# Kernel optimization log

Measured on AMD Instinct MI355X. Metric: run time of the kernel, lower is better.

The kernel has to match this reference:

```python
import jax, jax.numpy as jnp
import numpy as np

EPS = 1e-12  # F.normalize eps


def setup_inputs() -> dict:
    key = jax.random.key(0)
    k1, k2 = jax.random.split(key)
    bs, d = 8192, 128
    data = jax.random.normal(k1, (bs, d), dtype=jnp.float32)
    label = jax.random.randint(k2, (bs, 1), 0, 2, dtype=jnp.int64)
    scale = jnp.asarray(np.log(1.0 / 0.07), dtype=jnp.float32)  # learned temperature param
    return {"data": data, "scale": scale, "label": label}


def reference(data, scale, label):
    bs = data.shape[0]
    # L2-normalize rows (F.normalize semantics with eps clamp)
    norm = jnp.maximum(jnp.linalg.norm(data, axis=-1, keepdims=True), EPS)
    x = data / norm
    logits = (x @ x.T) * jnp.exp(scale)  # [bs, bs]
    # Vectorized equivalent of the python double loop: binary same-class matrix
    sim = (label == label.T).astype(logits.dtype)  # [bs, bs]
    q = jax.nn.softmax(sim / jnp.sum(sim, axis=-1, keepdims=True), axis=-1)
    p = jax.nn.log_softmax(logits, axis=-1)
    log_q = jnp.log(q)  # q > 0 always (softmax output)
    # F.kl_div(p, q, 'batchmean') = sum(q * (log q - p)) / bs
    loss1 = jnp.sum(q * (log_q - p)) / bs
    # F.kl_div(q.log(), p.exp(), 'batchmean') = sum(exp(p) * (p - log q)) / bs
    loss2 = jnp.sum(jnp.exp(p) * (p - log_q)) / bs
    return (loss1 + loss2) * 0.5
```

## Files before the change

### kernel.cpp

```cpp
#include <hip/hip_runtime.h>
#include <stdint.h>

#define BS 8192
#define DD 128
#define SPLIT 16

typedef __attribute__((ext_vector_type(8))) short short8;
typedef __attribute__((ext_vector_type(4))) float float4v;

#if __has_builtin(__builtin_amdgcn_exp2f)
#define EXP2(x) __builtin_amdgcn_exp2f(x)
#else
#define EXP2(x) exp2f(x)
#endif

__device__ __forceinline__ float bf2f(short s) {
  union { unsigned u; float f; } c;
  c.u = ((unsigned)(unsigned short)s) << 16;
  return c.f;
}
__device__ __forceinline__ short f2bf(float f) {
  union { float f; unsigned u; } c; c.f = f;
  unsigned u = c.u + 0x7FFFu + ((c.u >> 16) & 1u);
  return (short)(u >> 16);
}

__global__ __launch_bounds__(256) void k_norm(const float* __restrict__ data,
                                              const int* __restrict__ label,
                                              unsigned int* __restrict__ xnb32,
                                              float* __restrict__ xnf,
                                              float* __restrict__ gh,
                                              int* __restrict__ cnt,
                                              float* __restrict__ Zr,
                                              float* __restrict__ Ur,
                                              float* __restrict__ Vr,
                                              float* __restrict__ mf,
                                              float* __restrict__ out) {
  __shared__ float sh[256];
  __shared__ int shc[2];
  int tid = threadIdx.x, wave = tid >> 6, lane = tid & 63;
  if (tid < 2) shc[tid] = 0;
  sh[tid] = 0.f;
  if (tid < 32) {
    int row = blockIdx.x * 32 + tid;
    Zr[row] = 0.f; Ur[row] = 0.f; Vr[row] = 0.f;
    mf[row] = (label[row] == 0) ? 1.f : 0.f;
  }
  if (blockIdx.x == 0 && tid == 0) out[0] = 0.f;
  __syncthreads();
  float a00 = 0.f, a01 = 0.f, a10 = 0.f, a11 = 0.f;
  int c0 = 0, c1 = 0;
  int rbase = blockIdx.x * 32 + wave * 8;
  for (int r = 0; r < 8; ++r) {
    int row = rbase + r;
    float2 v = *(const float2*)&data[row * DD + lane * 2];
    float ss = v.x * v.x + v.y * v.y;
    for (int off = 32; off; off >>= 1) ss += __shfl_xor(ss, off);
    float rn = 1.f / fmaxf(sqrtf(ss), 1e-12f);
    float x0 = v.x * rn, x1 = v.y * rn;
    *(float2*)&xnf[row * DD + lane * 2] = make_float2(x0, x1);
    unsigned int pk = (unsigned int)(unsigned short)f2bf(x0) |
                      ((unsigned int)(unsigned short)f2bf(x1) << 16);
    xnb32[row * 64 + lane] = pk;
    int lab = label[row];
    if (lab == 0) { a00 += x0; a01 += x1; c0++; }
    else          { a10 += x0; a11 += x1; c1++; }
  }
  atomicAdd(&sh[2 * lane], a00);
  atomicAdd(&sh[2 * lane + 1], a01);
  atomicAdd(&sh[128 + 2 * lane], a10);
  atomicAdd(&sh[128 + 2 * lane + 1], a11);
  if (lane == 0) { atomicAdd(&shc[0], c0); atomicAdd(&shc[1], c1); }
  __syncthreads();
  atomicAdd(&gh[tid], sh[tid]);
  if (tid < 2) atomicAdd(&cnt[tid], shc[tid]);
}

__device__ __forceinline__ void stage_tile(const char* srcbase, int j0,
                                           char* dstbase, int tid) {
  int rowloc = tid >> 4;
  int swz = (tid & 15) ^ rowloc;
  char* dst = dstbase + tid * 16;
#pragma unroll
  for (int p = 0; p < 4; ++p) {
    const char* src = srcbase + (size_t)(j0 + p * 16 + rowloc) * 256 + swz * 16;
    __builtin_amdgcn_global_load_lds(
        (const __attribute__((address_space(1))) void*)(uintptr_t)src,
        (__attribute__((address_space(3))) void*)(uintptr_t)(dst + p * 4096), 16, 0, 0);
  }
}

__device__ __forceinline__ void consume_tile(const short* __restrict__ tile, int j0,
                                             const float* __restrict__ mf,
                                             const short8 afrag[2][4], int quad, int col,
                                             float Z[2][4], float U[2][4], float V0[2][4]) {
#pragma unroll
  for (int jo = 0; jo < 4; ++jo) {
    int jc = j0 + jo * 16 + col;
    float m0 = mf[jc];
    float4v c0 = {0.f, 0.f, 0.f, 0.f}, c1 = {0.f, 0.f, 0.f, 0.f};
    const short* bp = tile + (jo * 16 + col) * DD;
#pragma unroll
    for (int t = 0; t < 4; ++t) {
      short8 b = *(const short8*)(bp + ((t * 4 + quad) ^ col) * 8);
      c0 = __builtin_amdgcn_mfma_f32_16x16x32_bf16(afrag[0][t], b, c0, 0, 0, 0);
      c1 = __builtin_amdgcn_mfma_f32_16x16x32_bf16(afrag[1][t], b, c1, 0, 0, 0);
    }
#pragma unroll
    for (int r = 0; r < 4; ++r) {
      float l0 = c0[r], e0 = EXP2(l0);
      Z[0][r] += e0; U[0][r] += e0 * l0; V0[0][r] += m0 * e0;
      float l1 = c1[r], e1 = EXP2(l1);
      Z[1][r] += e1; U[1][r] += e1 * l1; V0[1][r] += m0 * e1;
    }
  }
}

__global__ __launch_bounds__(256) void k_main(const unsigned short* __restrict__ xnb,
                                              const int* __restrict__ label,
                                              const float* __restrict__ mf,
                                              const float* __restrict__ scale,
                                              float* __restrict__ Zr,
                                              float* __restrict__ Ur,
                                              float* __restrict__ Vr) {
  __shared__ short tileA[64 * DD];
  __shared__ short tileB[64 * DD];
  int tid = threadIdx.x, wave = tid >> 6, lane = tid & 63;
  int quad = lane >> 4, col = lane & 15;
  int rb = blockIdx.x / SPLIT, sl = blockIdx.x % SPLIT;
  float se2 = __expf(scale[0]) * 1.4426950408889634f;

  short8 afrag[2][4];
  int labI[2][4];
#pragma unroll
  for (int s = 0; s < 2; ++s) {
    int arow = rb * 128 + s * 64 + wave * 16 + col;
    const short* ap = (const short*)xnb + (size_t)arow * DD;
#pragma unroll
    for (int t = 0; t < 4; ++t) {
      short8 a = *(const short8*)(ap + t * 32 + quad * 8);
#pragma unroll
      for (int i = 0; i < 8; ++i) a[i] = f2bf(bf2f(a[i]) * se2);
      afrag[s][t] = a;
    }
#pragma unroll
    for (int r = 0; r < 4; ++r)
      labI[s][r] = label[rb * 128 + s * 64 + wave * 16 + quad * 4 + r];
  }

  float Z[2][4] = {}, U[2][4] = {}, V0[2][4] = {};

  const char* srcbase = (const char*)xnb;
  int jbase = sl * (BS / SPLIT), jend = jbase + (BS / SPLIT);

  stage_tile(srcbase, jbase, (char*)tileA, tid);
  __syncthreads();
  for (int j0 = jbase; j0 < jend; j0 += 128) {
    stage_tile(srcbase, j0 + 64, (char*)tileB, tid);
    consume_tile(tileA, j0, mf, afrag, quad, col, Z, U, V0);
    __syncthreads();
    int jn = (j0 + 128 < jend) ? (j0 + 128) : jbase;
    stage_tile(srcbase, jn, (char*)tileA, tid);
    consume_tile(tileB, j0 + 64, mf, afrag, quad, col, Z, U, V0);
    __syncthreads();
  }

#pragma unroll
  for (int s = 0; s < 2; ++s)
#pragma unroll
    for (int r = 0; r < 4; ++r)
#pragma unroll
      for (int off = 1; off < 16; off <<= 1) {
        Z[s][r] += __shfl_xor(Z[s][r], off);
        U[s][r] += __shfl_xor(U[s][r], off);
        V0[s][r] += __shfl_xor(V0[s][r], off);
      }
  if (col == 0) {
#pragma unroll
    for (int s = 0; s < 2; ++s)
#pragma unroll
      for (int r = 0; r < 4; ++r) {
        int row = rb * 128 + s * 64 + wave * 16 + quad * 4 + r;
        float v = (labI[s][r] == 0) ? V0[s][r] : (Z[s][r] - V0[s][r]);
        atomicAdd(&Zr[row], Z[s][r]);
        atomicAdd(&Ur[row], U[s][r] * 0.6931471805599453f);
        atomicAdd(&Vr[row], v);
      }
  }
}

__global__ __launch_bounds__(256) void k_final(const float* __restrict__ xnf,
                                               const int* __restrict__ label,
                                               const float* __restrict__ scale,
                                               const float* __restrict__ gh,
                                               const int* __restrict__ cnt,
                                               const float* __restrict__ Zr,
                                               const float* __restrict__ Ur,
                                               const float* __restrict__ Vr,
                                               float* __restrict__ out) {
  __shared__ float bsum[4];
  int tid = threadIdx.x, wave = tid >> 6, lane = tid & 63;
  float se = __expf(scale[0]);
  float h0a = gh[2 * lane], h0b = gh[2 * lane + 1];
  float h1a = gh[128 + 2 * lane], h1b = gh[128 + 2 * lane + 1];
  float ga = h0a + h1a, gb = h0b + h1b;
  float c0 = (float)cnt[0], c1 = (float)cnt[1];
  float local = 0.f;
  int rbase = blockIdx.x * 32 + wave * 8;
  for (int r = 0; r < 8; ++r) {
    int row = rbase + r;
    float2 x = *(const float2*)&xnf[row * DD + lane * 2];
    int lab = label[row];
    float sg = x.x * ga + x.y * gb;
    float sh_ = (lab == 0) ? (x.x * h0a + x.y * h0b) : (x.x * h1a + x.y * h1b);
    for (int off = 32; off; off >>= 1) {
      sg += __shfl_xor(sg, off);
      sh_ += __shfl_xor(sh_, off);
    }
    if (lane == 0) {
      float cc = (lab == 0) ? c0 : c1;
      float a = __expf(1.f / cc);
      float Zq = cc * a + ((float)BS - cc);
      float S = se * sg, T = se * sh_;
      float Z = Zr[row], U = Ur[row], V = Vr[row];
      local += a / Zq - (S + (a - 1.f) * T) / Zq + U / Z - V / (cc * Z);
    }
  }
  if (lane == 0) bsum[wave] = local;
  __syncthreads();
  if (tid == 0) {
    float s = bsum[0] + bsum[1] + bsum[2] + bsum[3];
    atomicAdd(out, s * (0.5f / (float)BS));
  }
}

extern "C" void kernel_launch(void* const* d_in, const int* in_sizes, int n_in,
                              void* d_out, int out_size, void* d_ws, size_t ws_size,
                              hipStream_t stream) {
  const float* data = (const float*)d_in[0];
  const float* scale = (const float*)d_in[1];
  const int* label = (const int*)d_in[2];
  char* ws = (char*)d_ws;
  unsigned short* xnb = (unsigned short*)ws;
  unsigned int* xnb32 = (unsigned int*)ws;
  float* xnf = (float*)(ws + 2097152);
  float* Zr = (float*)(ws + 6291456);
  float* Ur = (float*)(ws + 6324224);
  float* Vr = (float*)(ws + 6356992);
  float* gh = (float*)(ws + 6389760);
  int* cnt = (int*)(ws + 6390784);
  float* mf = (float*)(ws + 6390800);

  hipMemsetAsync(ws + 6389760, 0, 1032, stream);

  k_norm<<<256, 256, 0, stream>>>(data, label, xnb32, xnf, gh, cnt, Zr, Ur, Vr, mf,
                                  (float*)d_out);
  k_main<<<64 * SPLIT, 256, 0, stream>>>(xnb, label, mf, scale, Zr, Ur, Vr);
  k_final<<<256, 256, 0, stream>>>(xnf, label, scale, gh, cnt, Zr, Ur, Vr, (float*)d_out);
}
```

Before: 121.4 us.

## Exploit Gram matrix symmetry to compute each off-diagonal tile once

Since x@x.T is symmetric, the main kernel now computes only the upper-triangular set of 64x64 tile pairs (diagonal plus half of the circular offsets). Each off-diagonal tile adds both row sums and column sums, so the column-side partial Z/U/V values are reduced across quads and atomically added for the column rows. This roughly halves the MFMA and exp work. In exchange it adds more atomics, shuffles, a smaller A fragment per block, and a grid of 1152 blocks that each run less work.

```diff
diff --git a/kernel.cpp b/kernel.cpp
--- a/kernel.cpp
+++ b/kernel.cpp
@@ -3,7 +3,6 @@
 
 #define BS 8192
 #define DD 128
-#define SPLIT 16
 
 typedef __attribute__((ext_vector_type(8))) short short8;
 typedef __attribute__((ext_vector_type(4))) float float4v;
@@ -90,28 +89,42 @@
   }
 }
 
-__device__ __forceinline__ void consume_tile(const short* __restrict__ tile, int j0,
-                                             const float* __restrict__ mf,
-                                             const short8 afrag[2][4], int quad, int col,
-                                             float Z[2][4], float U[2][4], float V0[2][4]) {
+__device__ __forceinline__ void consume64(const short* __restrict__ tile, int jt64,
+                                          bool docol, const float* __restrict__ mf,
+                                          const short8 afrag[4], const float mrow[4],
+                                          int quad, int col,
+                                          float rZ[4], float rU[4], float rV[4],
+                                          float* __restrict__ Zr,
+                                          float* __restrict__ Ur,
+                                          float* __restrict__ Vr) {
 #pragma unroll
   for (int jo = 0; jo < 4; ++jo) {
-    int jc = j0 + jo * 16 + col;
-    float m0 = mf[jc];
-    float4v c0 = {0.f, 0.f, 0.f, 0.f}, c1 = {0.f, 0.f, 0.f, 0.f};
+    int jc = jt64 + jo * 16 + col;
+    float mcol = mf[jc];
+    float4v c = {0.f, 0.f, 0.f, 0.f};
     const short* bp = tile + (jo * 16 + col) * DD;
 #pragma unroll
     for (int t = 0; t < 4; ++t) {
       short8 b = *(const short8*)(bp + ((t * 4 + quad) ^ col) * 8);
-      c0 = __builtin_amdgcn_mfma_f32_16x16x32_bf16(afrag[0][t], b, c0, 0, 0, 0);
-      c1 = __builtin_amdgcn_mfma_f32_16x16x32_bf16(afrag[1][t], b, c1, 0, 0, 0);
-    }
+      c = __builtin_amdgcn_mfma_f32_16x16x32_bf16(afrag[t], b, c, 0, 0, 0);
+    }
+    float cZ = 0.f, cU = 0.f, cV = 0.f;
 #pragma unroll
     for (int r = 0; r < 4; ++r) {
-      float l0 = c0[r], e0 = EXP2(l0);
-      Z[0][r] += e0; U[0][r] += e0 * l0; V0[0][r] += m0 * e0;
-      float l1 = c1[r], e1 = EXP2(l1);
-      Z[1][r] += e1; U[1][r] += e1 * l1; V0[1][r] += m0 * e1;
+      float l = c[r], e = EXP2(l), el = e * l;
+      rZ[r] += e; rU[r] += el; rV[r] += mcol * e;
+      cZ += e; cU += el; cV += mrow[r] * e;
+    }
+    if (docol) {
+      cZ += __shfl_xor(cZ, 16); cZ += __shfl_xor(cZ, 32);
+      cU += __shfl_xor(cU, 16); cU += __shfl_xor(cU, 32);
+      cV += __shfl_xor(cV, 16); cV += __shfl_xor(cV, 32);
+      if (quad == 0) {
+        float vcol = (mcol > 0.5f) ? cV : (cZ - cV);
+        atomicAdd(&Zr[jc], cZ);
+        atomicAdd(&Ur[jc], cU * 0.6931471805599453f);
+        atomicAdd(&Vr[jc], vcol);
+      }
     }
   }
 }
@@ -127,65 +140,72 @@
   __shared__ short tileB[64 * DD];
   int tid = threadIdx.x, wave = tid >> 6, lane = tid & 63;
   int quad = lane >> 4, col = lane & 15;
-  int rb = blockIdx.x / SPLIT, sl = blockIdx.x % SPLIT;
+  int it = blockIdx.x / 9;
+  int sub = blockIdx.x % 9;
   float se2 = __expf(scale[0]) * 1.4426950408889634f;
 
-  short8 afrag[2][4];
-  int labI[2][4];
-#pragma unroll
-  for (int s = 0; s < 2; ++s) {
-    int arow = rb * 128 + s * 64 + wave * 16 + col;
-    const short* ap = (const short*)xnb + (size_t)arow * DD;
-#pragma unroll
-    for (int t = 0; t < 4; ++t) {
-      short8 a = *(const short8*)(ap + t * 32 + quad * 8);
-#pragma unroll
-      for (int i = 0; i < 8; ++i) a[i] = f2bf(bf2f(a[i]) * se2);
-      afrag[s][t] = a;
-    }
-#pragma unroll
-    for (int r = 0; r < 4; ++r)
-      labI[s][r] = label[rb * 128 + s * 64 + wave * 16 + quad * 4 + r];
-  }
-
-  float Z[2][4] = {}, U[2][4] = {}, V0[2][4] = {};
-
+  int rowbase = it * 64 + wave * 16;
+  const short* ap = (const short*)xnb + (size_t)(rowbase + col) * DD;
+  short8 afrag[4];
+#pragma unroll
+  for (int t = 0; t < 4; ++t) {
+    short8 a = *(const short8*)(ap + t * 32 + quad * 8);
+#pragma unroll
+    for (int i = 0; i < 8; ++i) a[i] = f2bf(bf2f(a[i]) * se2);
+    afrag[t] = a;
+  }
+  int labI[4];
+  float mrow[4];
+#pragma unroll
+  for (int r = 0; r < 4; ++r) {
+    int rr = rowbase + quad * 4 + r;
+    labI[r] = label[rr];
+    mrow[r] = mf[rr];
+  }
+
+  float rZ[4] = {}, rU[4] = {}, rV[4] = {};
   const char* srcbase = (const char*)xnb;
-  int jbase = sl * (BS / SPLIT), jend = jbase + (BS / SPLIT);
-
-  stage_tile(srcbase, jbase, (char*)tileA, tid);
-  __syncthreads();
-  for (int j0 = jbase; j0 < jend; j0 += 128) {
-    stage_tile(srcbase, j0 + 64, (char*)tileB, tid);
-    consume_tile(tileA, j0, mf, afrag, quad, col, Z, U, V0);
+
+  if (sub == 8) {
+    stage_tile(srcbase, it * 64, (char*)tileA, tid);
     __syncthreads();
-    int jn = (j0 + 128 < jend) ? (j0 + 128) : jbase;
-    stage_tile(srcbase, jn, (char*)tileA, tid);
-    consume_tile(tileB, j0 + 64, mf, afrag, quad, col, Z, U, V0);
+    consume64(tileA, it * 64, false, mf, afrag, mrow, quad, col, rZ, rU, rV, Zr, Ur, Vr);
+  } else {
+    int obase = sub * 8 + 1;
+    stage_tile(srcbase, ((it + obase) & 127) * 64, (char*)tileA, tid);
     __syncthreads();
-  }
-
-#pragma unroll
-  for (int s = 0; s < 2; ++s)
-#pragma unroll
-    for (int r = 0; r < 4; ++r)
-#pragma unroll
-      for (int off = 1; off < 16; off <<= 1) {
-        Z[s][r] += __shfl_xor(Z[s][r], off);
-        U[s][r] += __shfl_xor(U[s][r], off);
-        V0[s][r] += __shfl_xor(V0[s][r], off);
-      }
+    for (int p = 0; p < 8; p += 2) {
+      int jA = ((it + obase + p) & 127) * 64;
+      int jB = ((it + obase + p + 1) & 127) * 64;
+      int jN = ((it + obase + ((p + 2) & 7)) & 127) * 64;
+      stage_tile(srcbase, jB, (char*)tileB, tid);
+      if ((obase + p) < 64 || it < 64)
+        consume64(tileA, jA, true, mf, afrag, mrow, quad, col, rZ, rU, rV, Zr, Ur, Vr);
+      __syncthreads();
+      stage_tile(srcbase, jN, (char*)tileA, tid);
+      if ((obase + p + 1) < 64 || it < 64)
+        consume64(tileB, jB, true, mf, afrag, mrow, quad, col, rZ, rU, rV, Zr, Ur, Vr);
+      __syncthreads();
+    }
+  }
+
+#pragma unroll
+  for (int r = 0; r < 4; ++r)
+#pragma unroll
+    for (int off = 1; off < 16; off <<= 1) {
+      rZ[r] += __shfl_xor(rZ[r], off);
+      rU[r] += __shfl_xor(rU[r], off);
+      rV[r] += __shfl_xor(rV[r], off);
+    }
   if (col == 0) {
 #pragma unroll
-    for (int s = 0; s < 2; ++s)
-#pragma unroll
-      for (int r = 0; r < 4; ++r) {
-        int row = rb * 128 + s * 64 + wave * 16 + quad * 4 + r;
-        float v = (labI[s][r] == 0) ? V0[s][r] : (Z[s][r] - V0[s][r]);
-        atomicAdd(&Zr[row], Z[s][r]);
-        atomicAdd(&Ur[row], U[s][r] * 0.6931471805599453f);
-        atomicAdd(&Vr[row], v);
-      }
+    for (int r = 0; r < 4; ++r) {
+      int row = rowbase + quad * 4 + r;
+      float v = (labI[r] == 0) ? rV[r] : (rZ[r] - rV[r]);
+      atomicAdd(&Zr[row], rZ[r]);
+      atomicAdd(&Ur[row], rU[r] * 0.6931471805599453f);
+      atomicAdd(&Vr[row], v);
+    }
   }
 }
 
@@ -255,6 +275,6 @@
 
   k_norm<<<256, 256, 0, stream>>>(data, label, xnb32, xnf, gh, cnt, Zr, Ur, Vr, mf,
                                   (float*)d_out);
-  k_main<<<64 * SPLIT, 256, 0, stream>>>(xnb, label, mf, scale, Zr, Ur, Vr);
+  k_main<<<128 * 9, 256, 0, stream>>>(xnb, label, mf, scale, Zr, Ur, Vr);
   k_final<<<256, 256, 0, stream>>>(xnf, label, scale, gh, cnt, Zr, Ur, Vr, (float*)d_out);
 }
```

Result: slower. 141.2 us (+16.3%).
